# Kernel optimization log

Hardware: AMD Instinct MI355X
Metric: run time of the kernel (lower is better)

The kernel has to match this reference:

```python
import jax, jax.numpy as jnp
import numpy as np

B, N, M, D, H = 4, 512, 4096, 256, 8
HD = D // H


def setup_inputs() -> dict:
    key = jax.random.key(0)
    ks = jax.random.split(key, 10)
    s = 1.0 / np.sqrt(D)
    return {
        "amr_feats": jax.random.normal(ks[0], (B, N, D), jnp.float32),
        "amr_pad_mask": jax.random.randint(ks[1], (B, N), 0, 2) == 1,
        "visual_feats": jax.random.normal(ks[2], (B, M, D), jnp.float32),
        "W_amr_qk": jax.random.normal(ks[3], (D, D), jnp.float32) * s,
        "W_amr_v": jax.random.normal(ks[4], (D, D), jnp.float32) * s,
        "W_vis_qk": jax.random.normal(ks[5], (D, D), jnp.float32) * s,
        "W_vis_v": jax.random.normal(ks[6], (D, D), jnp.float32) * s,
        "W_amr_out": jax.random.normal(ks[7], (D, D), jnp.float32) * s,
        "b_amr_out": jnp.zeros((D,), jnp.float32),
        "W_vis_out": jax.random.normal(ks[8], (D, D), jnp.float32) * s,
        "b_vis_out": jnp.zeros((D,), jnp.float32),
    }


def _split_heads(x):  # [b, s, d] -> [b, h, s, hd]
    b, s, _ = x.shape
    return x.reshape(b, s, H, HD).transpose(0, 2, 1, 3)


def _merge_heads(x):  # [b, h, s, hd] -> [b, s, d]
    b, _, s, _ = x.shape
    return x.transpose(0, 2, 1, 3).reshape(b, s, H * HD)


def reference(amr_feats, amr_pad_mask, visual_feats,
              W_amr_qk, W_amr_v, W_vis_qk, W_vis_v,
              W_amr_out, b_amr_out, W_vis_out, b_vis_out):
    scale = HD ** -0.5
    amr_qk = _split_heads(amr_feats @ W_amr_qk)      # [b,h,n,hd]
    vis_qk = _split_heads(visual_feats @ W_vis_qk)   # [b,h,m,hd]
    amr_v = _split_heads(amr_feats @ W_amr_v)        # [b,h,n,hd]
    vis_v = _split_heads(visual_feats @ W_vis_v)     # [b,h,m,hd]

    # shared score matrix, computed once and reused for both directions
    common = jnp.einsum('bhnc,bhmc->bhnm', amr_qk, vis_qk) * scale  # [b,h,n,m]

    # amr -> visual (visual_pads is None in the top-level forward: no mask)
    amr_vis_w = jax.nn.softmax(common, axis=-1)
    amr_feats_2 = _merge_heads(jnp.einsum('bhnm,bhmc->bhnc', amr_vis_w, vis_v))
    amr_feats_2 = amr_feats_2 @ W_amr_out + b_amr_out

    # visual -> amr, masked by amr_pad_mask
    neg = jnp.finfo(common.dtype).min
    vis_txt = jnp.where(amr_pad_mask[:, None, None, :], neg,
                        common.transpose(0, 1, 3, 2))  # [b,h,m,n]
    vis_txt_w = jax.nn.softmax(vis_txt, axis=-1)
    visual_feats_2 = _merge_heads(jnp.einsum('bhmn,bhnc->bhmc', vis_txt_w, amr_v))
    visual_feats_2 = visual_feats_2 @ W_vis_out + b_vis_out

    # text_trans == 'dot', visual_trans == 'dot'
    return amr_feats_2 * amr_feats, visual_feats * visual_feats_2
```

## Files before the change

### kernel.cpp

```cpp
#include <hip/hip_runtime.h>

#define BB 4
#define NN 512
#define MM 4096
#define DD 256
#define HH 8
#define HDD 32

typedef __attribute__((ext_vector_type(8))) short bf16x8;
typedef __attribute__((ext_vector_type(4))) float f32x4;
typedef __attribute__((ext_vector_type(4))) unsigned int u32x4;

__device__ __forceinline__ unsigned short f2b(float f) {
    union { float f; unsigned u; } v; v.f = f;
    unsigned r = v.u + 0x7fffu + ((v.u >> 16) & 1u);
    return (unsigned short)(r >> 16);
}
__device__ __forceinline__ float b2f(unsigned short u) {
    union { unsigned u; float f; } v; v.u = ((unsigned)u) << 16;
    return v.f;
}
__device__ __forceinline__ unsigned cvt_pk_bf16(float lo, float hi) {
    unsigned r;
    asm("v_cvt_pk_bf16_f32 %0, %1, %2" : "=v"(r) : "v"(lo), "v"(hi));
    return r;
}

__global__ __launch_bounds__(256) void convert_feats(
    const float* __restrict__ amr, const float* __restrict__ vis,
    unsigned short* __restrict__ da, unsigned short* __restrict__ dv)
{
    const int bx = blockIdx.x;
    const float* s; unsigned short* d; int i;
    if (bx < 512) { s = amr; d = da; i = bx * 256 + threadIdx.x; }
    else          { s = vis; d = dv; i = (bx - 512) * 256 + threadIdx.x; }
    const float4 v = ((const float4*)s)[i];
    ushort4 o;
    o.x = f2b(v.x); o.y = f2b(v.y); o.z = f2b(v.z); o.w = f2b(v.w);
    ((ushort4*)d)[i] = o;
}

struct WPack { const float* s[6]; unsigned short* d[6]; };
__global__ __launch_bounds__(256) void convert_w(WPack p)
{
    const int mat = blockIdx.x >> 8;
    const int k = blockIdx.x & 255;
    const int c = threadIdx.x;
    p.d[mat][(size_t)c * DD + k] = f2b(p.s[mat][(size_t)k * DD + c]);
}

__global__ __launch_bounds__(256) void transpose_all(
    const unsigned short* __restrict__ visV,
    const unsigned short* __restrict__ amrV,
    unsigned short* __restrict__ VTv, unsigned short* __restrict__ VTa)
{
    const int bx = blockIdx.x;
    const unsigned short* X; unsigned short* VT; int SEQ, mb;
    if (bx < 16) { X = visV; VT = VTv; SEQ = MM; mb = bx; }
    else         { X = amrV; VT = VTa; SEQ = NN; mb = bx - 16; }
    const int m = mb * 256 + threadIdx.x;
    const int r = m & 31;
    const int p = ((r & 15) >> 2) * 8 + (r >> 4) * 4 + (r & 3);
    const int mstore = (m & ~31) | p;
    const int c0 = blockIdx.y * 8;
    const int b = blockIdx.z;
    const bf16x8 v = *(const bf16x8*)&X[((size_t)b * SEQ + m) * DD + c0];
    #pragma unroll
    for (int j = 0; j < 8; ++j)
        VT[((size_t)b * DD + c0 + j) * SEQ + mstore] = (unsigned short)v[j];
}

template<bool OUTPROJ>
__device__ __forceinline__ void gemm_tile(
    const unsigned short* __restrict__ A,
    const unsigned short* __restrict__ Wt,
    float outscale,
    const float* __restrict__ bias,
    const float* __restrict__ feats,
    unsigned short* __restrict__ Cb,
    float* __restrict__ Cf,
    int r0, int c0,
    unsigned short (*As)[72], unsigned short (*Ws)[72])
{
    const int tid = threadIdx.x;
    const int lane = tid & 63, w = tid >> 6;
    const int rq = (w >> 1) * 32, cq = (w & 1) * 32;
    const int srow = tid >> 2, skc = (tid & 3) * 16;
    const int g = lane >> 4, cl = lane & 15;

    f32x4 acc[2][2] = {};

    for (int ks = 0; ks < DD; ks += 64) {
        __syncthreads();
        {
            const unsigned short* ga = &A[(size_t)(r0 + srow) * DD + ks + skc];
            *(bf16x8*)&As[srow][skc]     = *(const bf16x8*)ga;
            *(bf16x8*)&As[srow][skc + 8] = *(const bf16x8*)(ga + 8);
            const unsigned short* gw = &Wt[(size_t)(c0 + srow) * DD + ks + skc];
            *(bf16x8*)&Ws[srow][skc]     = *(const bf16x8*)gw;
            *(bf16x8*)&Ws[srow][skc + 8] = *(const bf16x8*)(gw + 8);
        }
        __syncthreads();
        #pragma unroll
        for (int kh = 0; kh < 2; ++kh) {
            const int kk = kh * 32 + g * 8;
            const bf16x8 a0 = *(const bf16x8*)&As[rq + cl][kk];
            const bf16x8 a1 = *(const bf16x8*)&As[rq + 16 + cl][kk];
            const bf16x8 b0 = *(const bf16x8*)&Ws[cq + cl][kk];
            const bf16x8 b1 = *(const bf16x8*)&Ws[cq + 16 + cl][kk];
            acc[0][0] = __builtin_amdgcn_mfma_f32_16x16x32_bf16(a0, b0, acc[0][0], 0, 0, 0);
            acc[0][1] = __builtin_amdgcn_mfma_f32_16x16x32_bf16(a0, b1, acc[0][1], 0, 0, 0);
            acc[1][0] = __builtin_amdgcn_mfma_f32_16x16x32_bf16(a1, b0, acc[1][0], 0, 0, 0);
            acc[1][1] = __builtin_amdgcn_mfma_f32_16x16x32_bf16(a1, b1, acc[1][1], 0, 0, 0);
        }
    }

    #pragma unroll
    for (int sr = 0; sr < 2; ++sr)
    #pragma unroll
    for (int sc = 0; sc < 2; ++sc) {
        const int col = c0 + cq + sc * 16 + cl;
        #pragma unroll
        for (int reg = 0; reg < 4; ++reg) {
            const int row = r0 + rq + sr * 16 + g * 4 + reg;
            const size_t idx = (size_t)row * DD + col;
            if (OUTPROJ) {
                Cf[idx] = (acc[sr][sc][reg] + bias[col]) * feats[idx];
            } else {
                Cb[idx] = f2b(acc[sr][sc][reg] * outscale);
            }
        }
    }
}

struct InPack {
    const unsigned short* A[4];
    const unsigned short* Wt[4];
    unsigned short* C[4];
    float scale[4];
};
__global__ __launch_bounds__(256) void gemm_in(InPack p)
{
    __shared__ unsigned short As[64][72];
    __shared__ unsigned short Ws[64][72];
    const int bx = blockIdx.x;
    int which, rb;
    if (bx < 32)       { which = 0; rb = bx; }
    else if (bx < 64)  { which = 1; rb = bx - 32; }
    else if (bx < 320) { which = 2; rb = bx - 64; }
    else               { which = 3; rb = bx - 320; }
    gemm_tile<false>(p.A[which], p.Wt[which], p.scale[which], nullptr, nullptr,
                     p.C[which], nullptr, rb * 64, blockIdx.y * 64, As, Ws);
}

struct OutPack {
    const unsigned short* A[2];
    const unsigned short* Wt[2];
    const float* bias[2];
    const float* feats[2];
    float* O[2];
};
__global__ __launch_bounds__(256) void gemm_out(OutPack p)
{
    __shared__ unsigned short As[64][72];
    __shared__ unsigned short Ws[64][72];
    const int bx = blockIdx.x;
    const int which = (bx < 32) ? 0 : 1;
    const int rb = (bx < 32) ? bx : bx - 32;
    gemm_tile<true>(p.A[which], p.Wt[which], 1.f, p.bias[which], p.feats[which],
                    nullptr, p.O[which], rb * 64, blockIdx.y * 64, As, Ws);
}

template<int SEQK, int SPLIT, bool HAS_MASK>
__device__ __forceinline__ void attn_body(
    int bid,
    const unsigned short* __restrict__ Qb,
    const unsigned short* __restrict__ Kb,
    const unsigned short* __restrict__ VTb,
    const int* __restrict__ mask,
    unsigned short* __restrict__ ctx,
    float* __restrict__ Pl, unsigned short* __restrict__ PaccB,
    int NQ, float* maskadd)
{
    constexpr int KCHUNK = SEQK / SPLIT;
    constexpr int NT = KCHUNK / 64;

    const int tid = threadIdx.x;
    const int lane = tid & 63, w = tid >> 6;
    const int g = lane >> 4, cl = lane & 15;

    const int nqt = NQ / 256;
    int bi = bid;
    const int sp = bi % SPLIT; bi /= SPLIT;
    const int qt = bi % nqt;   bi /= nqt;
    const int h  = bi % HH;
    const int b  = bi / HH;
    const int q0 = qt * 256 + w * 64;
    const int kv0 = sp * KCHUNK;

    if (HAS_MASK) {
        for (int i = tid; i < SEQK; i += 256)
            maskadd[i] = mask[b * SEQK + i] ? -1e30f : 0.f;
        __syncthreads();
    }

    bf16x8 aq[4];
    #pragma unroll
    for (int qg = 0; qg < 4; ++qg)
        aq[qg] = *(const bf16x8*)
            &Qb[((size_t)b * NQ + q0 + qg * 16 + cl) * DD + h * HDD + g * 8];

    const unsigned short* Kp0 = Kb + (size_t)b * SEQK * DD + h * HDD + g * 8
                                   + (size_t)(kv0 + cl) * DD;
    const unsigned short* Vp0 = VTb + ((size_t)b * DD + h * HDD + cl) * SEQK
                                    + kv0 + g * 8;

    float lsum[4] = {0.f, 0.f, 0.f, 0.f};
    f32x4 acc[4][2] = {};

    bf16x8 Kc[4], Kn[4];
    #pragma unroll
    for (int kf = 0; kf < 4; ++kf)
        Kc[kf] = *(const bf16x8*)(Kp0 + (size_t)(kf * 16) * DD);

    for (int t = 0; t < NT; ++t) {
        const int m0 = kv0 + t * 64;

        if (t + 1 < NT) {
            const unsigned short* kp = Kp0 + (size_t)((t + 1) * 64) * DD;
            #pragma unroll
            for (int kf = 0; kf < 4; ++kf)
                Kn[kf] = *(const bf16x8*)(kp + (size_t)(kf * 16) * DD);
        }

        bf16x8 vv[2][2];
        #pragma unroll
        for (int mh = 0; mh < 2; ++mh)
            #pragma unroll
            for (int sub = 0; sub < 2; ++sub)
                vv[mh][sub] = *(const bf16x8*)
                    (Vp0 + (size_t)(sub * 16) * SEQK + t * 64 + mh * 32);

        uint2 X[4][4];
        #pragma unroll
        for (int kh = 0; kh < 2; ++kh) {
            f32x4 s[4][2];
            #pragma unroll
            for (int k2 = 0; k2 < 2; ++k2) {
                const f32x4 z = {0.f, 0.f, 0.f, 0.f};
                const bf16x8 kfrag = Kc[kh * 2 + k2];
                #pragma unroll
                for (int qg = 0; qg < 4; ++qg)
                    s[qg][k2] = __builtin_amdgcn_mfma_f32_16x16x32_bf16(
                        kfrag, aq[qg], z, 0, 0, 0);
            }
            #pragma unroll
            for (int k2 = 0; k2 < 2; ++k2) {
                const int kf = kh * 2 + k2;
                f32x4 madd;
                if (HAS_MASK)
                    madd = *(const f32x4*)&maskadd[m0 + kf * 16 + g * 4];
                #pragma unroll
                for (int qg = 0; qg < 4; ++qg) {
                    const float p0 = exp2f(s[qg][k2][0] + (HAS_MASK ? madd[0] : 0.f));
                    const float p1 = exp2f(s[qg][k2][1] + (HAS_MASK ? madd[1] : 0.f));
                    const float p2 = exp2f(s[qg][k2][2] + (HAS_MASK ? madd[2] : 0.f));
                    const float p3 = exp2f(s[qg][k2][3] + (HAS_MASK ? madd[3] : 0.f));
                    lsum[qg] += (p0 + p1) + (p2 + p3);
                    X[qg][kf].x = cvt_pk_bf16(p0, p1);
                    X[qg][kf].y = cvt_pk_bf16(p2, p3);
                }
            }
        }

        #pragma unroll
        for (int mh = 0; mh < 2; ++mh) {
            union { u32x4 u; bf16x8 b; } pa[4];
            #pragma unroll
            for (int qg = 0; qg < 4; ++qg) {
                pa[qg].u[0] = X[qg][mh * 2].x;
                pa[qg].u[1] = X[qg][mh * 2].y;
                pa[qg].u[2] = X[qg][mh * 2 + 1].x;
                pa[qg].u[3] = X[qg][mh * 2 + 1].y;
            }
            #pragma unroll
            for (int sub = 0; sub < 2; ++sub)
                #pragma unroll
                for (int qg = 0; qg < 4; ++qg)
                    acc[qg][sub] = __builtin_amdgcn_mfma_f32_16x16x32_bf16(
                        pa[qg].b, vv[mh][sub], acc[qg][sub], 0, 0, 0);
        }

        #pragma unroll
        for (int kf = 0; kf < 4; ++kf) Kc[kf] = Kn[kf];
    }

    #pragma unroll
    for (int qg = 0; qg < 4; ++qg) {
        lsum[qg] += __shfl_xor(lsum[qg], 16);
        lsum[qg] += __shfl_xor(lsum[qg], 32);
    }

    if (SPLIT > 1) {
        const int pb = bid;
        #pragma unroll
        for (int qg = 0; qg < 4; ++qg) {
            #pragma unroll
            for (int sub = 0; sub < 2; ++sub)
                #pragma unroll
                for (int reg = 0; reg < 4; ++reg) {
                    const int wq = w * 64 + qg * 16 + g * 4 + reg;
                    PaccB[((size_t)pb * 256 + wq) * 32 + sub * 16 + cl]
                        = f2b(acc[qg][sub][reg]);
                }
            if (g == 0)
                Pl[(size_t)pb * 256 + w * 64 + qg * 16 + cl] = lsum[qg];
        }
    } else {
        float linv[4][4];
        #pragma unroll
        for (int qg = 0; qg < 4; ++qg)
            #pragma unroll
            for (int reg = 0; reg < 4; ++reg)
                linv[qg][reg] = __shfl(lsum[qg], g * 4 + reg);
        #pragma unroll
        for (int qg = 0; qg < 4; ++qg)
            #pragma unroll
            for (int sub = 0; sub < 2; ++sub)
                #pragma unroll
                for (int reg = 0; reg < 4; ++reg) {
                    const int q = q0 + qg * 16 + g * 4 + reg;
                    ctx[((size_t)b * NQ + q) * DD + h * HDD + sub * 16 + cl]
                        = f2b(acc[qg][sub][reg] / linv[qg][reg]);
                }
    }
}

__global__ __launch_bounds__(256) void attn_fused(
    const unsigned short* __restrict__ amr_qk,
    const unsigned short* __restrict__ vis_qk,
    const unsigned short* __restrict__ VT_vis,
    const unsigned short* __restrict__ VT_amr,
    const int* __restrict__ mask,
    unsigned short* __restrict__ ctx1,
    float* __restrict__ Pl, unsigned short* __restrict__ PaccB)
{
    __shared__ float maskadd[NN];
    if ((blockIdx.x & 1) == 0) {
        attn_body<MM, 8, false>(blockIdx.x >> 1, amr_qk, vis_qk, VT_vis, nullptr,
                                nullptr, Pl, PaccB, NN, maskadd);
    } else {
        attn_body<NN, 1, true>(blockIdx.x >> 1, vis_qk, amr_qk, VT_amr, mask,
                               ctx1, nullptr, nullptr, MM, maskadd);
    }
}

__global__ __launch_bounds__(256) void combine_split(
    const float* __restrict__ Pl, const unsigned short* __restrict__ PaccB,
    unsigned short* __restrict__ ctx)
{
    const int q = threadIdx.x;
    const int bqt = blockIdx.x;
    const int qt = bqt & 1, h = (bqt >> 1) & 7, b = bqt >> 4;
    const int pb0 = bqt * 8;

    float denom = 0.f;
    float o[32] = {};
    #pragma unroll
    for (int sp = 0; sp < 8; ++sp) {
        const size_t base = ((size_t)(pb0 + sp) * 256 + q) * 32;
        #pragma unroll
        for (int c8 = 0; c8 < 4; ++c8) {
            const bf16x8 a = *(const bf16x8*)&PaccB[base + c8 * 8];
            #pragma unroll
            for (int j = 0; j < 8; ++j)
                o[c8 * 8 + j] += b2f((unsigned short)a[j]);
        }
        denom += Pl[(size_t)(pb0 + sp) * 256 + q];
    }
    const float inv = 1.f / denom;

    unsigned short* dst = &ctx[((size_t)b * NN + qt * 256 + q) * DD + h * HDD];
    #pragma unroll
    for (int j4 = 0; j4 < 8; ++j4) {
        ushort4 u;
        u.x = f2b(o[j4 * 4 + 0] * inv); u.y = f2b(o[j4 * 4 + 1] * inv);
        u.z = f2b(o[j4 * 4 + 2] * inv); u.w = f2b(o[j4 * 4 + 3] * inv);
        *(ushort4*)(dst + j4 * 4) = u;
    }
}

extern "C" void kernel_launch(void* const* d_in, const int* in_sizes, int n_in,
                              void* d_out, int out_size, void* d_ws, size_t ws_size,
                              hipStream_t stream)
{
    const float* amr_feats    = (const float*)d_in[0];
    const int*   amr_pad_mask = (const int*)d_in[1];
    const float* visual_feats = (const float*)d_in[2];
    const float* W_amr_qk     = (const float*)d_in[3];
    const float* W_amr_v      = (const float*)d_in[4];
    const float* W_vis_qk     = (const float*)d_in[5];
    const float* W_vis_v      = (const float*)d_in[6];
    const float* W_amr_out    = (const float*)d_in[7];
    const float* b_amr_out    = (const float*)d_in[8];
    const float* W_vis_out    = (const float*)d_in[9];
    const float* b_vis_out    = (const float*)d_in[10];

    unsigned short* ws = (unsigned short*)d_ws;
    unsigned short* amr_fb     = ws;
    unsigned short* vis_fb     = ws + 524288;
    unsigned short* Wt_amr_qk  = ws + 4718592;
    unsigned short* Wt_amr_v   = ws + 4784128;
    unsigned short* Wt_vis_qk  = ws + 4849664;
    unsigned short* Wt_vis_v   = ws + 4915200;
    unsigned short* Wt_amr_out = ws + 4980736;
    unsigned short* Wt_vis_out = ws + 5046272;
    unsigned short* amr_qk_b   = ws + 5111808;
    unsigned short* amr_v_b    = ws + 5636096;
    unsigned short* vis_qk_b   = ws + 6160384;
    unsigned short* vis_v_b    = ws + 10354688;
    unsigned short* ctx0_b     = ws + 14548992;
    unsigned short* ctx1_b     = ws + 15073280;
    unsigned short* VT_vis     = ws + 19267584;
    unsigned short* VT_amr     = ws + 23461888;
    float* Pl             = (float*)ws;
    unsigned short* PaccB = ws + 262144;

    float* out0 = (float*)d_out;
    float* out1 = out0 + (size_t)BB * NN * DD;

    const float SQS = 0.50500976f;

    convert_feats<<<4608, 256, 0, stream>>>(amr_feats, visual_feats, amr_fb, vis_fb);
    WPack wp;
    wp.s[0] = W_amr_qk;  wp.d[0] = Wt_amr_qk;
    wp.s[1] = W_amr_v;   wp.d[1] = Wt_amr_v;
    wp.s[2] = W_vis_qk;  wp.d[2] = Wt_vis_qk;
    wp.s[3] = W_vis_v;   wp.d[3] = Wt_vis_v;
    wp.s[4] = W_amr_out; wp.d[4] = Wt_amr_out;
    wp.s[5] = W_vis_out; wp.d[5] = Wt_vis_out;
    convert_w<<<1536, 256, 0, stream>>>(wp);

    InPack ip;
    ip.A[0] = amr_fb; ip.Wt[0] = Wt_amr_qk; ip.C[0] = amr_qk_b; ip.scale[0] = SQS;
    ip.A[1] = amr_fb; ip.Wt[1] = Wt_amr_v;  ip.C[1] = amr_v_b;  ip.scale[1] = 1.f;
    ip.A[2] = vis_fb; ip.Wt[2] = Wt_vis_qk; ip.C[2] = vis_qk_b; ip.scale[2] = SQS;
    ip.A[3] = vis_fb; ip.Wt[3] = Wt_vis_v;  ip.C[3] = vis_v_b;  ip.scale[3] = 1.f;
    gemm_in<<<dim3(576, 4), 256, 0, stream>>>(ip);

    transpose_all<<<dim3(18, 32, 4), 256, 0, stream>>>(vis_v_b, amr_v_b, VT_vis, VT_amr);

    attn_fused<<<1024, 256, 0, stream>>>(
        amr_qk_b, vis_qk_b, VT_vis, VT_amr, amr_pad_mask, ctx1_b, Pl, PaccB);
    combine_split<<<64, 256, 0, stream>>>(Pl, PaccB, ctx0_b);

    OutPack op;
    op.A[0] = ctx0_b; op.Wt[0] = Wt_amr_out; op.bias[0] = b_amr_out;
    op.feats[0] = amr_feats;    op.O[0] = out0;
    op.A[1] = ctx1_b; op.Wt[1] = Wt_vis_out; op.bias[1] = b_vis_out;
    op.feats[1] = visual_feats; op.O[1] = out1;
    gemm_out<<<dim3(288, 4), 256, 0, stream>>>(op);
}
```

Measured before the change: 105.6 us.

## Fuse feature conversion and V transpose into input GEMM, split attention finer

Removes the separate fp32-to-bf16 feature conversion kernel and the V transpose kernel. The input GEMM now loads fp32 activations and converts them in registers, and its V-projection epilogue writes the permuted transposed layout directly through shared memory. The weight conversion becomes a 64x64 tiled transpose through shared memory with coalesced accesses. The amr->visual attention split goes from 8 to 16 chunks, which adds more blocks and a larger combine reduction. The goal is fewer launches, less intermediate global traffic and better occupancy, at the cost of more combine work.

```diff
diff --git a/kernel.cpp b/kernel.cpp
--- a/kernel.cpp
+++ b/kernel.cpp
@@ -26,59 +26,38 @@
     return r;
 }
 
-__global__ __launch_bounds__(256) void convert_feats(
-    const float* __restrict__ amr, const float* __restrict__ vis,
-    unsigned short* __restrict__ da, unsigned short* __restrict__ dv)
-{
-    const int bx = blockIdx.x;
-    const float* s; unsigned short* d; int i;
-    if (bx < 512) { s = amr; d = da; i = bx * 256 + threadIdx.x; }
-    else          { s = vis; d = dv; i = (bx - 512) * 256 + threadIdx.x; }
-    const float4 v = ((const float4*)s)[i];
-    ushort4 o;
-    o.x = f2b(v.x); o.y = f2b(v.y); o.z = f2b(v.z); o.w = f2b(v.w);
-    ((ushort4*)d)[i] = o;
-}
-
 struct WPack { const float* s[6]; unsigned short* d[6]; };
 __global__ __launch_bounds__(256) void convert_w(WPack p)
 {
-    const int mat = blockIdx.x >> 8;
-    const int k = blockIdx.x & 255;
-    const int c = threadIdx.x;
-    p.d[mat][(size_t)c * DD + k] = f2b(p.s[mat][(size_t)k * DD + c]);
-}
-
-__global__ __launch_bounds__(256) void transpose_all(
-    const unsigned short* __restrict__ visV,
-    const unsigned short* __restrict__ amrV,
-    unsigned short* __restrict__ VTv, unsigned short* __restrict__ VTa)
-{
-    const int bx = blockIdx.x;
-    const unsigned short* X; unsigned short* VT; int SEQ, mb;
-    if (bx < 16) { X = visV; VT = VTv; SEQ = MM; mb = bx; }
-    else         { X = amrV; VT = VTa; SEQ = NN; mb = bx - 16; }
-    const int m = mb * 256 + threadIdx.x;
-    const int r = m & 31;
-    const int p = ((r & 15) >> 2) * 8 + (r >> 4) * 4 + (r & 3);
-    const int mstore = (m & ~31) | p;
-    const int c0 = blockIdx.y * 8;
-    const int b = blockIdx.z;
-    const bf16x8 v = *(const bf16x8*)&X[((size_t)b * SEQ + m) * DD + c0];
-    #pragma unroll
-    for (int j = 0; j < 8; ++j)
-        VT[((size_t)b * DD + c0 + j) * SEQ + mstore] = (unsigned short)v[j];
-}
-
-template<bool OUTPROJ>
-__device__ __forceinline__ void gemm_tile(
-    const unsigned short* __restrict__ A,
+    __shared__ unsigned short T[64][72];
+    const int mat = blockIdx.x >> 4;
+    const int tile = blockIdx.x & 15;
+    const int kt = (tile >> 2) * 64, ct = (tile & 3) * 64;
+    const int t = threadIdx.x;
+    const int kl = t >> 2, cseg = (t & 3) * 16;
+
+    const float* src = &p.s[mat][(size_t)(kt + kl) * DD + ct + cseg];
+    #pragma unroll
+    for (int j4 = 0; j4 < 4; ++j4) {
+        const float4 f = *(const float4*)(src + j4 * 4);
+        T[cseg + j4 * 4 + 0][kl] = f2b(f.x);
+        T[cseg + j4 * 4 + 1][kl] = f2b(f.y);
+        T[cseg + j4 * 4 + 2][kl] = f2b(f.z);
+        T[cseg + j4 * 4 + 3][kl] = f2b(f.w);
+    }
+    __syncthreads();
+    unsigned short* dst = &p.d[mat][(size_t)(ct + kl) * DD + kt + cseg];
+    *(bf16x8*)dst       = *(const bf16x8*)&T[kl][cseg];
+    *(bf16x8*)(dst + 8) = *(const bf16x8*)&T[kl][cseg + 8];
+}
+
+template<int OUTMODE>
+__device__ __forceinline__ void gemm_tile_in(
+    const float* __restrict__ A,
     const unsigned short* __restrict__ Wt,
     float outscale,
-    const float* __restrict__ bias,
-    const float* __restrict__ feats,
     unsigned short* __restrict__ Cb,
-    float* __restrict__ Cf,
+    unsigned short* __restrict__ VT, int SEQ,
     int r0, int c0,
     unsigned short (*As)[72], unsigned short (*Ws)[72])
 {
@@ -93,9 +72,18 @@
     for (int ks = 0; ks < DD; ks += 64) {
         __syncthreads();
         {
-            const unsigned short* ga = &A[(size_t)(r0 + srow) * DD + ks + skc];
-            *(bf16x8*)&As[srow][skc]     = *(const bf16x8*)ga;
-            *(bf16x8*)&As[srow][skc + 8] = *(const bf16x8*)(ga + 8);
+            const float* ga = &A[(size_t)(r0 + srow) * DD + ks + skc];
+            const float4 f0 = *(const float4*)(ga);
+            const float4 f1 = *(const float4*)(ga + 4);
+            const float4 f2 = *(const float4*)(ga + 8);
+            const float4 f3 = *(const float4*)(ga + 12);
+            uint4 u0, u1;
+            u0.x = cvt_pk_bf16(f0.x, f0.y); u0.y = cvt_pk_bf16(f0.z, f0.w);
+            u0.z = cvt_pk_bf16(f1.x, f1.y); u0.w = cvt_pk_bf16(f1.z, f1.w);
+            u1.x = cvt_pk_bf16(f2.x, f2.y); u1.y = cvt_pk_bf16(f2.z, f2.w);
+            u1.z = cvt_pk_bf16(f3.x, f3.y); u1.w = cvt_pk_bf16(f3.z, f3.w);
+            *(uint4*)&As[srow][skc]     = u0;
+            *(uint4*)&As[srow][skc + 8] = u1;
             const unsigned short* gw = &Wt[(size_t)(c0 + srow) * DD + ks + skc];
             *(bf16x8*)&Ws[srow][skc]     = *(const bf16x8*)gw;
             *(bf16x8*)&Ws[srow][skc + 8] = *(const bf16x8*)(gw + 8);
@@ -115,6 +103,103 @@
         }
     }
 
+    if (OUTMODE == 0) {
+        #pragma unroll
+        for (int sr = 0; sr < 2; ++sr)
+        #pragma unroll
+        for (int sc = 0; sc < 2; ++sc) {
+            const int col = c0 + cq + sc * 16 + cl;
+            #pragma unroll
+            for (int reg = 0; reg < 4; ++reg) {
+                const int row = r0 + rq + sr * 16 + g * 4 + reg;
+                Cb[(size_t)row * DD + col] = f2b(acc[sr][sc][reg] * outscale);
+            }
+        }
+    } else {
+        __syncthreads();
+        #pragma unroll
+        for (int sr = 0; sr < 2; ++sr)
+        #pragma unroll
+        for (int sc = 0; sc < 2; ++sc) {
+            const int col_local = cq + sc * 16 + cl;
+            uint2 u;
+            u.x = cvt_pk_bf16(acc[sr][sc][0], acc[sr][sc][1]);
+            u.y = cvt_pk_bf16(acc[sr][sc][2], acc[sr][sc][3]);
+            *(uint2*)&As[col_local][rq + g * 8 + sr * 4] = u;
+        }
+        __syncthreads();
+        const int col = tid >> 2, seg = tid & 3;
+        const int b = r0 / SEQ, m0 = r0 % SEQ;
+        unsigned short* dst = &VT[((size_t)b * DD + c0 + col) * SEQ + m0 + seg * 16];
+        *(bf16x8*)dst       = *(const bf16x8*)&As[col][seg * 16];
+        *(bf16x8*)(dst + 8) = *(const bf16x8*)&As[col][seg * 16 + 8];
+    }
+}
+
+struct InPack {
+    const float* amr; const float* vis;
+    const unsigned short *Wqa, *Wva, *Wqv, *Wvv;
+    unsigned short *amr_qk, *vis_qk, *VTa, *VTv;
+    float sqs;
+};
+__global__ __launch_bounds__(256) void gemm_in(InPack p)
+{
+    __shared__ unsigned short As[64][72];
+    __shared__ unsigned short Ws[64][72];
+    const int bx = blockIdx.x;
+    const int c0 = blockIdx.y * 64;
+    if (bx < 32)
+        gemm_tile_in<0>(p.amr, p.Wqa, p.sqs, p.amr_qk, nullptr, 0, bx * 64, c0, As, Ws);
+    else if (bx < 64)
+        gemm_tile_in<2>(p.amr, p.Wva, 1.f, nullptr, p.VTa, NN, (bx - 32) * 64, c0, As, Ws);
+    else if (bx < 320)
+        gemm_tile_in<0>(p.vis, p.Wqv, p.sqs, p.vis_qk, nullptr, 0, (bx - 64) * 64, c0, As, Ws);
+    else
+        gemm_tile_in<2>(p.vis, p.Wvv, 1.f, nullptr, p.VTv, MM, (bx - 320) * 64, c0, As, Ws);
+}
+
+__device__ __forceinline__ void gemm_tile_out(
+    const unsigned short* __restrict__ A,
+    const unsigned short* __restrict__ Wt,
+    const float* __restrict__ bias,
+    const float* __restrict__ feats,
+    float* __restrict__ Cf,
+    int r0, int c0,
+    unsigned short (*As)[72], unsigned short (*Ws)[72])
+{
+    const int tid = threadIdx.x;
+    const int lane = tid & 63, w = tid >> 6;
+    const int rq = (w >> 1) * 32, cq = (w & 1) * 32;
+    const int srow = tid >> 2, skc = (tid & 3) * 16;
+    const int g = lane >> 4, cl = lane & 15;
+
+    f32x4 acc[2][2] = {};
+
+    for (int ks = 0; ks < DD; ks += 64) {
+        __syncthreads();
+        {
+            const unsigned short* ga = &A[(size_t)(r0 + srow) * DD + ks + skc];
+            *(bf16x8*)&As[srow][skc]     = *(const bf16x8*)ga;
+            *(bf16x8*)&As[srow][skc + 8] = *(const bf16x8*)(ga + 8);
+            const unsigned short* gw = &Wt[(size_t)(c0 + srow) * DD + ks + skc];
+            *(bf16x8*)&Ws[srow][skc]     = *(const bf16x8*)gw;
+            *(bf16x8*)&Ws[srow][skc + 8] = *(const bf16x8*)(gw + 8);
+        }
+        __syncthreads();
+        #pragma unroll
+        for (int kh = 0; kh < 2; ++kh) {
+            const int kk = kh * 32 + g * 8;
+            const bf16x8 a0 = *(const bf16x8*)&As[rq + cl][kk];
+            const bf16x8 a1 = *(const bf16x8*)&As[rq + 16 + cl][kk];
+            const bf16x8 b0 = *(const bf16x8*)&Ws[cq + cl][kk];
+            const bf16x8 b1 = *(const bf16x8*)&Ws[cq + 16 + cl][kk];
+            acc[0][0] = __builtin_amdgcn_mfma_f32_16x16x32_bf16(a0, b0, acc[0][0], 0, 0, 0);
+            acc[0][1] = __builtin_amdgcn_mfma_f32_16x16x32_bf16(a0, b1, acc[0][1], 0, 0, 0);
+            acc[1][0] = __builtin_amdgcn_mfma_f32_16x16x32_bf16(a1, b0, acc[1][0], 0, 0, 0);
+            acc[1][1] = __builtin_amdgcn_mfma_f32_16x16x32_bf16(a1, b1, acc[1][1], 0, 0, 0);
+        }
+    }
+
     #pragma unroll
     for (int sr = 0; sr < 2; ++sr)
     #pragma unroll
@@ -124,33 +209,9 @@
         for (int reg = 0; reg < 4; ++reg) {
             const int row = r0 + rq + sr * 16 + g * 4 + reg;
             const size_t idx = (size_t)row * DD + col;
-            if (OUTPROJ) {
-                Cf[idx] = (acc[sr][sc][reg] + bias[col]) * feats[idx];
-            } else {
-                Cb[idx] = f2b(acc[sr][sc][reg] * outscale);
-            }
-        }
-    }
-}
-
-struct InPack {
-    const unsigned short* A[4];
-    const unsigned short* Wt[4];
-    unsigned short* C[4];
-    float scale[4];
-};
-__global__ __launch_bounds__(256) void gemm_in(InPack p)
-{
-    __shared__ unsigned short As[64][72];
-    __shared__ unsigned short Ws[64][72];
-    const int bx = blockIdx.x;
-    int which, rb;
-    if (bx < 32)       { which = 0; rb = bx; }
-    else if (bx < 64)  { which = 1; rb = bx - 32; }
-    else if (bx < 320) { which = 2; rb = bx - 64; }
-    else               { which = 3; rb = bx - 320; }
-    gemm_tile<false>(p.A[which], p.Wt[which], p.scale[which], nullptr, nullptr,
-                     p.C[which], nullptr, rb * 64, blockIdx.y * 64, As, Ws);
+            Cf[idx] = (acc[sr][sc][reg] + bias[col]) * feats[idx];
+        }
+    }
 }
 
 struct OutPack {
@@ -167,8 +228,8 @@
     const int bx = blockIdx.x;
     const int which = (bx < 32) ? 0 : 1;
     const int rb = (bx < 32) ? bx : bx - 32;
-    gemm_tile<true>(p.A[which], p.Wt[which], 1.f, p.bias[which], p.feats[which],
-                    nullptr, p.O[which], rb * 64, blockIdx.y * 64, As, Ws);
+    gemm_tile_out(p.A[which], p.Wt[which], p.bias[which], p.feats[which],
+                  p.O[which], rb * 64, blockIdx.y * 64, As, Ws);
 }
 
 template<int SEQK, int SPLIT, bool HAS_MASK>
@@ -346,11 +407,12 @@
     float* __restrict__ Pl, unsigned short* __restrict__ PaccB)
 {
     __shared__ float maskadd[NN];
-    if ((blockIdx.x & 1) == 0) {
-        attn_body<MM, 8, false>(blockIdx.x >> 1, amr_qk, vis_qk, VT_vis, nullptr,
-                                nullptr, Pl, PaccB, NN, maskadd);
+    const int group = blockIdx.x / 3, rem = blockIdx.x % 3;
+    if (rem < 2) {
+        attn_body<MM, 16, false>(group * 2 + rem, amr_qk, vis_qk, VT_vis, nullptr,
+                                 nullptr, Pl, PaccB, NN, maskadd);
     } else {
-        attn_body<NN, 1, true>(blockIdx.x >> 1, vis_qk, amr_qk, VT_amr, mask,
+        attn_body<NN, 1, true>(group, vis_qk, amr_qk, VT_amr, mask,
                                ctx1, nullptr, nullptr, MM, maskadd);
     }
 }
@@ -362,12 +424,12 @@
     const int q = threadIdx.x;
     const int bqt = blockIdx.x;
     const int qt = bqt & 1, h = (bqt >> 1) & 7, b = bqt >> 4;
-    const int pb0 = bqt * 8;
+    const int pb0 = bqt * 16;
 
     float denom = 0.f;
     float o[32] = {};
     #pragma unroll
-    for (int sp = 0; sp < 8; ++sp) {
+    for (int sp = 0; sp < 16; ++sp) {
         const size_t base = ((size_t)(pb0 + sp) * 256 + q) * 32;
         #pragma unroll
         for (int c8 = 0; c8 < 4; ++c8) {
@@ -407,31 +469,26 @@
     const float* b_vis_out    = (const float*)d_in[10];
 
     unsigned short* ws = (unsigned short*)d_ws;
-    unsigned short* amr_fb     = ws;
-    unsigned short* vis_fb     = ws + 524288;
-    unsigned short* Wt_amr_qk  = ws + 4718592;
-    unsigned short* Wt_amr_v   = ws + 4784128;
-    unsigned short* Wt_vis_qk  = ws + 4849664;
-    unsigned short* Wt_vis_v   = ws + 4915200;
-    unsigned short* Wt_amr_out = ws + 4980736;
-    unsigned short* Wt_vis_out = ws + 5046272;
-    unsigned short* amr_qk_b   = ws + 5111808;
-    unsigned short* amr_v_b    = ws + 5636096;
-    unsigned short* vis_qk_b   = ws + 6160384;
-    unsigned short* vis_v_b    = ws + 10354688;
-    unsigned short* ctx0_b     = ws + 14548992;
-    unsigned short* ctx1_b     = ws + 15073280;
-    unsigned short* VT_vis     = ws + 19267584;
-    unsigned short* VT_amr     = ws + 23461888;
-    float* Pl             = (float*)ws;
-    unsigned short* PaccB = ws + 262144;
+    unsigned short* Wt_amr_qk  = ws;
+    unsigned short* Wt_amr_v   = ws + 65536;
+    unsigned short* Wt_vis_qk  = ws + 131072;
+    unsigned short* Wt_vis_v   = ws + 196608;
+    unsigned short* Wt_amr_out = ws + 262144;
+    unsigned short* Wt_vis_out = ws + 327680;
+    unsigned short* amr_qk_b   = ws + 393216;
+    unsigned short* VT_amr     = ws + 917504;
+    unsigned short* vis_qk_b   = ws + 1441792;
+    unsigned short* VT_vis     = ws + 5636096;
+    unsigned short* ctx0_b     = ws + 9830400;
+    unsigned short* ctx1_b     = ws + 10354688;
+    float* Pl                  = (float*)(ws + 14548992);
+    unsigned short* PaccB      = ws + 15073280;
 
     float* out0 = (float*)d_out;
     float* out1 = out0 + (size_t)BB * NN * DD;
 
     const float SQS = 0.50500976f;
 
-    convert_feats<<<4608, 256, 0, stream>>>(amr_feats, visual_feats, amr_fb, vis_fb);
     WPack wp;
     wp.s[0] = W_amr_qk;  wp.d[0] = Wt_amr_qk;
     wp.s[1] = W_amr_v;   wp.d[1] = Wt_amr_v;
@@ -439,18 +496,18 @@
     wp.s[3] = W_vis_v;   wp.d[3] = Wt_vis_v;
     wp.s[4] = W_amr_out; wp.d[4] = Wt_amr_out;
     wp.s[5] = W_vis_out; wp.d[5] = Wt_vis_out;
-    convert_w<<<1536, 256, 0, stream>>>(wp);
+    convert_w<<<96, 256, 0, stream>>>(wp);
 
     InPack ip;
-    ip.A[0] = amr_fb; ip.Wt[0] = Wt_amr_qk; ip.C[0] = amr_qk_b; ip.scale[0] = SQS;
-    ip.A[1] = amr_fb; ip.Wt[1] = Wt_amr_v;  ip.C[1] = amr_v_b;  ip.scale[1] = 1.f;
-    ip.A[2] = vis_fb; ip.Wt[2] = Wt_vis_qk; ip.C[2] = vis_qk_b; ip.scale[2] = SQS;
-    ip.A[3] = vis_fb; ip.Wt[3] = Wt_vis_v;  ip.C[3] = vis_v_b;  ip.scale[3] = 1.f;
+    ip.amr = amr_feats; ip.vis = visual_feats;
+    ip.Wqa = Wt_amr_qk; ip.Wva = Wt_amr_v;
+    ip.Wqv = Wt_vis_qk; ip.Wvv = Wt_vis_v;
+    ip.amr_qk = amr_qk_b; ip.vis_qk = vis_qk_b;
+    ip.VTa = VT_amr; ip.VTv = VT_vis;
+    ip.sqs = SQS;
     gemm_in<<<dim3(576, 4), 256, 0, stream>>>(ip);
 
-    transpose_all<<<dim3(18, 32, 4), 256, 0, stream>>>(vis_v_b, amr_v_b, VT_vis, VT_amr);
-
-    attn_fused<<<1024, 256, 0, stream>>>(
+    attn_fused<<<1536, 256, 0, stream>>>(
         amr_qk_b, vis_qk_b, VT_vis, VT_amr, amr_pad_mask, ctx1_b, Pl, PaccB);
     combine_split<<<64, 256, 0, stream>>>(Pl, PaccB, ctx0_b);
 
```

Result: slower. 108.2 us (+2.4%).
